# Kernel optimization log

Measured on AMD Instinct MI355X. Metric: run time of the kernel, lower is better.

The kernel has to match this reference:

```python
import jax, jax.numpy as jnp
import numpy as np

# iRPE contextual+transposed, method=PRODUCT, rpe config ratio=1.9
ALPHA, BETA, GAMMA = 1.9, 3.8, 15.2
BETA_INT = int(BETA)            # 3
S = 2 * BETA_INT + 1            # 7
NUM_BUCKETS = S * S             # 49
B, H, D = 8, 8, 64
HEIGHT = WIDTH = 32
L = HEIGHT * WIDTH              # 1024, skip = L - height*width = 0


def _piecewise_index(rp):
    # numpy port of torch piecewise_index (no-grad, precomputed constant)
    rp = np.asarray(rp)
    rp_abs = np.abs(rp)
    safe = np.maximum(rp_abs.astype(np.float64), ALPHA)  # avoid log(0) under mask
    y = ALPHA + np.log(safe / ALPHA) / np.log(GAMMA / ALPHA) * (BETA - ALPHA)
    y = np.minimum(np.round(y), BETA)                    # round then clip(max=beta)
    out = np.where(rp_abs <= ALPHA, np.round(rp.astype(np.float64)), np.sign(rp) * y)
    return out.astype(np.int64)                          # trunc toward zero (+-3.8 -> +-3)


def _rp_bucket_product(height, width):
    pos = np.stack(np.meshgrid(np.arange(height), np.arange(width), indexing='ij'), -1)
    pos = pos.reshape(-1, 2)                             # (L, 2)
    diff = pos[:, None, :] - pos[None, :, :]             # (L, L, 2)
    r = _piecewise_index(diff[:, :, 0]) + BETA_INT
    c = _piecewise_index(diff[:, :, 1]) + BETA_INT
    return (r * S + c).astype(np.int32)                  # values in [0, 49)


def setup_inputs() -> dict:
    key = jax.random.key(0)
    k1, k2 = jax.random.split(key)
    x = jax.random.normal(k1, (B, H, L, D), dtype=jnp.float32)
    lookup_table_weight = jax.random.normal(k2, (H, D, NUM_BUCKETS), dtype=jnp.float32) * 0.02
    rp_bucket = jnp.asarray(_rp_bucket_product(HEIGHT, WIDTH))  # (L, L) int32 constant
    return {"x": x, "lookup_table_weight": lookup_table_weight, "rp_bucket": rp_bucket}


def reference(x, lookup_table_weight, rp_bucket):
    # x: (B, H, L, D); lookup_table_weight: (H, D, K); rp_bucket: (L, L) int
    # lt[b,h,l,k] = sum_d x[b,h,l,d] * W[h,d,k]
    lt = jnp.einsum('bhld,hdk->bhlk', x, lookup_table_weight)  # (B, H, L, K) small
    Lq = rp_bucket.shape[0]
    row = jnp.arange(Lq)[:, None]                              # (L, 1)
    # out[b,h,i,j] = lt[b,h,i,rp_bucket[i,j]] -- the big irregular gather
    return lt[:, :, row, rp_bucket]                            # (B, H, L, L)
```

## Files before the change

### kernel.cpp

```cpp
#include <hip/hip_runtime.h>


constexpr int cL = 1024;
constexpr int cD = 64;
constexpr int cK = 49;

typedef float vf4 __attribute__((ext_vector_type(4)));

__global__ __launch_bounds__(512, 4) void irpe_fused(
    const float* __restrict__ x,
    const float* __restrict__ W,
    const int*   __restrict__ bucket,
    float*       __restrict__ out)
{
    __shared__ float sc[8][64];

    const int gid  = blockIdx.x;
    const int i    = ((gid & 255) << 2) | (gid >> 8);
    const int tid  = threadIdx.x;
    const int lane = tid & 63;
    const int w    = tid >> 6;

    const int kc = lane < cK ? lane : (cK - 1);
    const float* wb = W + (size_t)w * cD * cK + kc;
    float wr[cD];
    #pragma unroll
    for (int d = 0; d < cD; ++d)
        wr[d] = wb[(size_t)d * cK];

    const int4* brow = (const int4*)(bucket + (size_t)i * cL);

    for (int q = 0; q < 8; ++q) {
        const int bh = q * 8 + w;

        const float* xr = x + ((size_t)bh * cL + i) * cD;
        float acc = 0.0f;
        #pragma unroll
        for (int d = 0; d < cD; ++d)
            acc = fmaf(xr[d], wr[d], acc);

        sc[w][lane] = acc;

        vf4* orow = (vf4*)(out + ((size_t)bh * cL + i) * cL);
        #pragma unroll
        for (int t = 0; t < 4; ++t) {
            const int4 bk = brow[t * 64 + lane];
            const float* s = sc[w];
            vf4 o;
            o.x = s[bk.x];
            o.y = s[bk.y];
            o.z = s[bk.z];
            o.w = s[bk.w];
            __builtin_nontemporal_store(o, &orow[t * 64 + lane]);
        }
    }
}

extern "C" void kernel_launch(void* const* d_in, const int* in_sizes, int n_in,
                              void* d_out, int out_size, void* d_ws, size_t ws_size,
                              hipStream_t stream) {
    const float* x      = (const float*)d_in[0];
    const float* W      = (const float*)d_in[1];
    const int*   bucket = (const int*)d_in[2];
    float*       out    = (float*)d_out;

    irpe_fused<<<cL, 512, 0, stream>>>(x, W, bucket, out);
}
```

Before: 331.9 us.

## Pre-transpose W and split rows across half-blocks with vectorized dot products

Adds a small kernel that transposes the lookup weight into a (H,K,D) layout in workspace, so each lane reads its weight column contiguously as float4 instead of keeping 64 strided values in registers. The main kernel now uses 256-thread blocks, each handling 32 of the 64 batch-head pairs for a row, with twice as many blocks and a different row-to-block mapping. The x row offset is made wave-uniform so it can be a scalar load. This trades register pressure and per-block W preloading for repeated per-iteration W reads from cache and an extra kernel launch.

```diff
diff --git a/kernel.cpp b/kernel.cpp
--- a/kernel.cpp
+++ b/kernel.cpp
@@ -7,45 +7,63 @@
 
 typedef float vf4 __attribute__((ext_vector_type(4)));
 
-__global__ __launch_bounds__(512, 4) void irpe_fused(
+__global__ void transpose_w(const float* __restrict__ W, float* __restrict__ Wt) {
+    const int hk = blockIdx.x;
+    const int d  = threadIdx.x;
+    const int h  = hk / cK;
+    const int k  = hk - h * cK;
+    Wt[(size_t)hk * cD + d] = W[((size_t)h * cD + d) * cK + k];
+}
+
+__global__ __launch_bounds__(256) void irpe_fused(
     const float* __restrict__ x,
-    const float* __restrict__ W,
+    const float* __restrict__ Wt,
     const int*   __restrict__ bucket,
     float*       __restrict__ out)
 {
-    __shared__ float sc[8][64];
+    __shared__ float sc[4][64];
 
     const int gid  = blockIdx.x;
-    const int i    = ((gid & 255) << 2) | (gid >> 8);
+    const int i_lo = gid >> 8;
+    const int rest = gid & 255;
+    const int i_hi = rest >> 1;
+    const int half = gid & 1;
+    const int i    = i_hi * 8 + i_lo;
+    const int bh0  = half * 32;
     const int tid  = threadIdx.x;
     const int lane = tid & 63;
     const int w    = tid >> 6;
 
     const int kc = lane < cK ? lane : (cK - 1);
-    const float* wb = W + (size_t)w * cD * cK + kc;
-    float wr[cD];
-    #pragma unroll
-    for (int d = 0; d < cD; ++d)
-        wr[d] = wb[(size_t)d * cK];
-
     const int4* brow = (const int4*)(bucket + (size_t)i * cL);
 
     for (int q = 0; q < 8; ++q) {
-        const int bh = q * 8 + w;
+        const int lh = q * 4 + w;
+        const int bh = bh0 + lh;
+        const int h  = bh & 7;
 
-        const float* xr = x + ((size_t)bh * cL + i) * cD;
+        const int xoff = __builtin_amdgcn_readfirstlane((bh * cL + i) * cD);
+        const vf4* xr4 = (const vf4*)(x + xoff);
+        const vf4* wr4 = (const vf4*)(Wt + ((size_t)h * cK + kc) * cD);
+
         float acc = 0.0f;
         #pragma unroll
-        for (int d = 0; d < cD; ++d)
-            acc = fmaf(xr[d], wr[d], acc);
+        for (int d4 = 0; d4 < cD / 4; ++d4) {
+            const vf4 xv = xr4[d4];
+            const vf4 wv = wr4[d4];
+            acc = fmaf(xv.x, wv.x, acc);
+            acc = fmaf(xv.y, wv.y, acc);
+            acc = fmaf(xv.z, wv.z, acc);
+            acc = fmaf(xv.w, wv.w, acc);
+        }
 
         sc[w][lane] = acc;
+        const float* s = sc[w];
 
         vf4* orow = (vf4*)(out + ((size_t)bh * cL + i) * cL);
         #pragma unroll
         for (int t = 0; t < 4; ++t) {
             const int4 bk = brow[t * 64 + lane];
-            const float* s = sc[w];
             vf4 o;
             o.x = s[bk.x];
             o.y = s[bk.y];
@@ -63,6 +81,8 @@
     const float* W      = (const float*)d_in[1];
     const int*   bucket = (const int*)d_in[2];
     float*       out    = (float*)d_out;
+    float*       Wt     = (float*)d_ws;
 
-    irpe_fused<<<cL, 512, 0, stream>>>(x, W, bucket, out);
+    transpose_w<<<8 * cK, cD, 0, stream>>>(W, Wt);
+    irpe_fused<<<cL * 2, 256, 0, stream>>>(x, Wt, bucket, out);
 }
```

Result: no change. 336.7 us (+1.5%).
